# Kernel tuning notes

Measured on AMD Instinct MI355X. Metric: run time of the kernel, lower is better.

## Reference

```python
import jax, jax.numpy as jnp
import numpy as np
from jax import lax

B, S, H, T = 64, 512, 1024, 17


def setup_inputs() -> dict:
    key = jax.random.key(0)
    ks = jax.random.split(key, 7)
    x = jax.random.normal(ks[0], (B, S, H), dtype=jnp.float32)
    W = jax.random.normal(ks[1], (T, H), dtype=jnp.float32) * 0.02
    b = jax.random.normal(ks[2], (T,), dtype=jnp.float32) * 0.02
    transitions = jax.random.normal(ks[3], (T, T), dtype=jnp.float32)
    start_trans = jax.random.normal(ks[4], (T,), dtype=jnp.float32)
    end_trans = jax.random.normal(ks[5], (T,), dtype=jnp.float32)
    nwords = jax.random.randint(ks[6], (B,), 1, S + 1, dtype=jnp.int32)
    return {"x": x, "W": W, "b": b, "transitions": transitions,
            "start_trans": start_trans, "end_trans": end_trans, "nwords": nwords}


def _viterbi(feats, mask_bs, transitions, start_trans, end_trans):
    # feats: [B,S,T]; mask_bs: [B,S] bool. Returns best tag sequence [B,S] (int32).
    Bt, St, Tt = feats.shape
    init = start_trans[None, :] + feats[:, 0]  # [B,T]
    idT = jnp.arange(Tt, dtype=jnp.int32)

    def step(score, inp):
        f_t, m_t = inp  # [B,T], [B]
        cand = score[:, :, None] + transitions[None, :, :]      # [B,Tprev,Tcur]
        best = jnp.max(cand, axis=1) + f_t                      # [B,T]
        bp = jnp.argmax(cand, axis=1).astype(jnp.int32)         # [B,T]
        m = m_t[:, None]
        new_score = jnp.where(m, best, score)
        bp = jnp.where(m, bp, idT[None, :])                     # identity where padded
        return new_score, bp

    xs = (jnp.swapaxes(feats[:, 1:], 0, 1), jnp.swapaxes(mask_bs[:, 1:], 0, 1))
    final, bps = lax.scan(step, init, xs)                       # bps: [S-1,B,T]
    final = final + end_trans[None, :]
    last_tag = jnp.argmax(final, axis=1).astype(jnp.int32)      # [B]

    def back(tag, bp_t):
        prev = jnp.take_along_axis(bp_t, tag[:, None], axis=1)[:, 0]
        return prev, tag

    first_tag, later_tags = lax.scan(back, last_tag, bps, reverse=True)
    tags = jnp.concatenate([first_tag[:, None], jnp.swapaxes(later_tags, 0, 1)], axis=1)  # [B,S]
    return tags


def reference(x, W, b, transitions, start_trans, end_trans, nwords):
    # dropout p=0.0 -> identity
    feats = jnp.einsum('bsh,th->bst', x, W) + b                 # hidden2tag
    mask_bs = jnp.arange(feats.shape[1])[None, :] < nwords[:, None]
    tags = _viterbi(feats, mask_bs, transitions, start_trans, end_trans)
    padded_tags = jnp.where(mask_bs, tags, 0).astype(jnp.float32)  # pad=0, float dtype
    return padded_tags, feats
```

## Files before the change

### kernel.cpp

```cpp
#include <hip/hip_runtime.h>

#define HDIM 1024
#define TDIM 17
#define BDIM 64
#define SDIM 512
#define NROWS (BDIM * SDIM)
#define NCH 8
#define CHL 64

__global__ __launch_bounds__(256) void gemm_kernel(
    const float* __restrict__ x, const float* __restrict__ W,
    const float* __restrict__ bias, float* __restrict__ feats) {
  __shared__ __align__(16) float sW[TDIM * 512];
  int tid = threadIdx.x;
  int sub = tid & 15;
  int g = tid >> 4;
  int row0 = blockIdx.x * 32 + g * 2;
  const float* xr = x + (size_t)row0 * HDIM;
  float acc[2][TDIM];
#pragma unroll
  for (int r = 0; r < 2; ++r)
#pragma unroll
    for (int t = 0; t < TDIM; ++t) acc[r][t] = 0.f;

  for (int ph = 0; ph < 2; ++ph) {
    if (ph) __syncthreads();
    for (int i = tid; i < TDIM * 128; i += 256) {
      int t = i >> 7;
      int k = (i & 127) * 4;
      *(float4*)&sW[t * 512 + k] =
          *(const float4*)&W[(size_t)t * HDIM + ph * 512 + k];
    }
    __syncthreads();
    float4 xv[2], xn[2];
#pragma unroll
    for (int r = 0; r < 2; ++r)
      xv[r] = *(const float4*)(xr + r * HDIM + ph * 512 + sub * 4);
#pragma unroll
    for (int c = 0; c < 8; ++c) {
      if (c < 7) {
#pragma unroll
        for (int r = 0; r < 2; ++r)
          xn[r] =
              *(const float4*)(xr + r * HDIM + ph * 512 + (c + 1) * 64 + sub * 4);
      }
#pragma unroll
      for (int t = 0; t < TDIM; ++t) {
        float4 wv = *(const float4*)&sW[t * 512 + c * 64 + sub * 4];
#pragma unroll
        for (int r = 0; r < 2; ++r) {
          float a = acc[r][t];
          a = fmaf(xv[r].x, wv.x, a);
          a = fmaf(xv[r].y, wv.y, a);
          a = fmaf(xv[r].z, wv.z, a);
          a = fmaf(xv[r].w, wv.w, a);
          acc[r][t] = a;
        }
      }
#pragma unroll
      for (int r = 0; r < 2; ++r) xv[r] = xn[r];
    }
  }
#pragma unroll
  for (int r = 0; r < 2; ++r)
#pragma unroll
    for (int t = 0; t < TDIM; ++t) {
#pragma unroll
      for (int m = 1; m < 16; m <<= 1)
        acc[r][t] += __shfl_xor(acc[r][t], m, 64);
    }
#pragma unroll
  for (int r = 0; r < 2; ++r) {
    float val = acc[r][0];
#pragma unroll
    for (int t = 1; t < 16; ++t) val = (sub == t) ? acc[r][t] : val;
    feats[(size_t)(row0 + r) * TDIM + sub] = val + bias[sub];
    if (sub == 0)
      feats[(size_t)(row0 + r) * TDIM + 16] = acc[r][16] + bias[16];
  }
}

__device__ __forceinline__ float vmax17(const float* v) {
  float m0 = fmaxf(fmaxf(v[0], v[1]), v[2]);
  float m1 = fmaxf(fmaxf(v[3], v[4]), v[5]);
  float m2 = fmaxf(fmaxf(v[6], v[7]), v[8]);
  float m3 = fmaxf(fmaxf(v[9], v[10]), v[11]);
  float m4 = fmaxf(fmaxf(v[12], v[13]), v[14]);
  float m5 = fmaxf(v[15], v[16]);
  float n0 = fmaxf(fmaxf(m0, m1), m2);
  float n1 = fmaxf(fmaxf(m3, m4), m5);
  return fmaxf(n0, n1);
}

__global__ __launch_bounds__(384) void chunkprod_kernel(
    const float* __restrict__ feats, const float* __restrict__ trans,
    const int* __restrict__ nwords, float* __restrict__ Pbuf) {
  int bc = blockIdx.x;
  int b = bc >> 3, c = bc & 7;
  int nw = nwords[b];
  if (nw < 1) nw = 1;
  if (nw > SDIM) nw = SDIM;
  if (c > 0 && c * CHL > nw - 1) return;
  int tid = threadIdx.x;
  int wid = tid >> 6, lane = tid & 63;
  int g = lane / 17, j = lane % 17;
  int gc = g < 3 ? g : 2;
  int e = wid * 3 + gc;
  int ibase = gc * 17 * 4;
  const float* fb = feats + (size_t)b * SDIM * TDIM;
  float tcol[TDIM];
#pragma unroll
  for (int i = 0; i < TDIM; ++i) tcol[i] = trans[i * TDIM + j];
  float s = (j == e) ? 0.f : -1e30f;
  int t_start = (c == 0) ? 1 : c * CHL;
  int t_end = c * CHL + CHL - 1;
  if (t_end > nw - 1) t_end = nw - 1;
  int tA = t_start;
  int tB = t_start + 1;
  if (tB > t_end) tB = t_start;
  float fA = fb[(size_t)tA * TDIM + j];
  float fB = fb[(size_t)tB * TDIM + j];
  for (int t = t_start; t <= t_end; ++t) {
    int t2 = t + 2;
    if (t2 > t_end) t2 = t_end;
    float fC = fb[(size_t)t2 * TDIM + j];
    int sb = __float_as_int(s);
    float v[TDIM];
#pragma unroll
    for (int i = 0; i < TDIM; ++i)
      v[i] = __int_as_float(__builtin_amdgcn_ds_bpermute(ibase + 4 * i, sb)) +
             tcol[i];
    float maxv = vmax17(v);
    s = maxv + fA;
    fA = fB;
    fB = fC;
  }
  if (g < 3 && e < TDIM)
    Pbuf[((size_t)(b * NCH + c) * TDIM + e) * TDIM + j] = s;
}

__global__ __launch_bounds__(64) void scan_kernel(
    const float* __restrict__ feats, const float* __restrict__ start_t,
    const float* __restrict__ end_t, const int* __restrict__ nwords,
    const float* __restrict__ Pbuf, float* __restrict__ bnd,
    int* __restrict__ elast) {
  int b = blockIdx.x;
  int lane = threadIdx.x;
  int jj = lane < TDIM ? lane : TDIM - 1;
  int nw = nwords[b];
  if (nw < 1) nw = 1;
  if (nw > SDIM) nw = SDIM;
  int clast = (nw - 1) >> 6;
  float w = start_t[jj] + feats[(size_t)b * SDIM * TDIM + jj];
  for (int c = 0; c <= clast; ++c) {
    const float* Pc = Pbuf + (size_t)(b * NCH + c) * TDIM * TDIM;
    float pj[TDIM];
#pragma unroll
    for (int i = 0; i < TDIM; ++i) pj[i] = Pc[i * TDIM + jj];
    int wb = __float_as_int(w);
    float v[TDIM];
#pragma unroll
    for (int i = 0; i < TDIM; ++i)
      v[i] = __int_as_float(__builtin_amdgcn_ds_bpermute(4 * i, wb)) + pj[i];
    w = vmax17(v);
    if (lane < TDIM) bnd[(b * NCH + c) * TDIM + lane] = w;
  }
  float fin = w + end_t[jj];
  float tmax = (lane < TDIM) ? fin : -1e30f;
#pragma unroll
  for (int m = 1; m < 64; m <<= 1) tmax = fmaxf(tmax, __shfl_xor(tmax, m, 64));
  unsigned long long mm = __ballot(fin == tmax) & 0x1FFFFull;
  if (lane == 0) elast[b] = (int)(__ffsll((unsigned long long)mm) - 1);
}

__global__ __launch_bounds__(64) void rerun_kernel(
    const float* __restrict__ feats, const float* __restrict__ trans,
    const float* __restrict__ start_t, const int* __restrict__ nwords,
    const float* __restrict__ bnd, int* __restrict__ etag,
    unsigned* __restrict__ seq32) {
  __shared__ unsigned char s_bp[CHL * 20];
  __shared__ __align__(4) unsigned char s_seq[TDIM * 68];
  int bc = blockIdx.x;
  int b = bc >> 3, c = bc & 7;
  int nw = nwords[b];
  if (nw < 1) nw = 1;
  if (nw > SDIM) nw = SDIM;
  if (c > 0 && c * CHL > nw - 1) return;
  int lane = threadIdx.x;
  int jj = lane < TDIM ? lane : TDIM - 1;
  const float* fb = feats + (size_t)b * SDIM * TDIM;
  float tcol[TDIM];
#pragma unroll
  for (int i = 0; i < TDIM; ++i) tcol[i] = trans[i * TDIM + jj];
  float sj = (c == 0) ? (start_t[jj] + fb[jj])
                      : bnd[(b * NCH + c - 1) * TDIM + jj];
  int t_start = (c == 0) ? 1 : c * CHL;
  int t_end = c * CHL + CHL - 1;
  if (t_end > nw - 1) t_end = nw - 1;
  int tA = t_start;
  int tB = t_start + 1;
  if (tB > t_end) tB = t_start;
  float fA = fb[(size_t)tA * TDIM + jj];
  float fB = fb[(size_t)tB * TDIM + jj];
  for (int t = t_start; t <= t_end; ++t) {
    int t2 = t + 2;
    if (t2 > t_end) t2 = t_end;
    float fC = fb[(size_t)t2 * TDIM + jj];
    int sb = __float_as_int(sj);
    float v[TDIM];
#pragma unroll
    for (int i = 0; i < TDIM; ++i)
      v[i] = __int_as_float(__builtin_amdgcn_ds_bpermute(4 * i, sb)) + tcol[i];
    float maxv = vmax17(v);
    unsigned msk = 0;
#pragma unroll
    for (int i = 0; i < TDIM; ++i) msk |= (v[i] == maxv) ? (1u << i) : 0u;
    int bp = __ffs(msk) - 1;
    s_bp[(t - c * CHL) * 20 + jj] = (unsigned char)bp;
    sj = maxv + fA;
    fA = fB;
    fB = fC;
  }
  __syncthreads();
  if (lane < TDIM) {
    int tag = lane;
    for (int t = t_end; t >= t_start; --t) {
      int u = t - c * CHL;
      s_seq[lane * 68 + u] = (unsigned char)tag;
      tag = s_bp[u * 20 + tag];
    }
    if (c == 0)
      s_seq[lane * 68 + 0] = (unsigned char)tag;
    else
      etag[(b * NCH + c) * TDIM + lane] = tag;
  }
  __syncthreads();
  for (int i = lane; i < TDIM * 16; i += 64) {
    int e2 = i >> 4, q = i & 15;
    seq32[(((size_t)(b * NCH + c) * TDIM + e2) << 4) + q] =
        *(const unsigned*)&s_seq[e2 * 68 + q * 4];
  }
}

__global__ __launch_bounds__(64) void stitch_kernel(
    const int* __restrict__ nwords, const int* __restrict__ elast,
    const int* __restrict__ etag, const unsigned* __restrict__ seq32,
    float* __restrict__ tags_out) {
  __shared__ unsigned long long stz[64];
  int b = blockIdx.x;
  int lane = threadIdx.x;
  int nw = nwords[b];
  if (nw < 1) nw = 1;
  if (nw > SDIM) nw = SDIM;
  stz[lane] = 0ull;
  __syncthreads();
  unsigned char* st = (unsigned char*)stz;
  int clast = (nw - 1) >> 6;
  int e = elast[b];
  for (int c = clast; c >= 0; --c) {
    int t_end = c * CHL + CHL - 1;
    if (t_end > nw - 1) t_end = nw - 1;
    int u_end = t_end - c * CHL;
    if (lane < 16) {
      unsigned wv = seq32[(((size_t)(b * NCH + c) * TDIM + e) << 4) + lane];
#pragma unroll
      for (int z = 0; z < 4; ++z) {
        int u = lane * 4 + z;
        if (u <= u_end) st[c * CHL + u] = (wv >> (8 * z)) & 0xff;
      }
    }
    if (c > 0) e = etag[(b * NCH + c) * TDIM + e];
  }
  __syncthreads();
  float* ob = tags_out + (size_t)b * SDIM;
  for (int t = lane; t < SDIM; t += 64)
    ob[t] = (t < nw) ? (float)st[t] : 0.f;
}

#define TRS 20
#define MVC 136

__global__ __launch_bounds__(64) void viterbi_kernel(
    const float* __restrict__ feats, const float* __restrict__ trans,
    const float* __restrict__ start_t, const float* __restrict__ end_t,
    const int* __restrict__ nwords, float* __restrict__ tags_out) {
  __shared__ __align__(16) float s_mv[64 * MVC];
  __shared__ float s_tr[TDIM * TRS];
  __shared__ unsigned char s_tags[SDIM];
  int b = blockIdx.x;
  int lane = threadIdx.x;
  const float* fb = feats + (size_t)b * SDIM * TDIM;
  for (int i = lane; i < TDIM * TDIM; i += 64)
    s_tr[(i / TDIM) * TRS + (i % TDIM)] = trans[i];
  __syncthreads();
  int nw = nwords[b];
  if (nw < 1) nw = 1;
  if (nw > SDIM) nw = SDIM;
  int jj = lane < TDIM ? lane : TDIM - 1;
  float tcol[TDIM];
#pragma unroll
  for (int i = 0; i < TDIM; ++i) tcol[i] = trans[i * TDIM + jj];
  float s[TDIM];
#pragma unroll
  for (int i = 0; i < TDIM; ++i) s[i] = start_t[i] + fb[i];
  float s0reg = start_t[jj] + fb[jj];
  auto load8g = [&](float* f, int t) {
#pragma unroll
    for (int u = 0; u < 8; ++u) f[u] = fb[(size_t)(t + u) * TDIM + jj];
  };
  auto step = [&](float fcu) -> float {
    float v[TDIM];
#pragma unroll
    for (int i = 0; i < TDIM; ++i) v[i] = s[i] + tcol[i];
    float maxv = vmax17(v);
    float ns = maxv + fcu;
#pragma unroll
    for (int i = 0; i < TDIM; ++i)
      s[i] = __uint_as_float(
          (unsigned)__builtin_amdgcn_readlane((int)__float_as_uint(ns), i));
    return maxv;
  };
  float fc[8], fn[8], mvr[8];
  load8g(fc, 0);
  {
    load8g(fn, 8);
    mvr[0] = 0.f;
#pragma unroll
    for (int u = 1; u < 8; ++u) {
      mvr[u] = 0.f;
      if (u < nw) mvr[u] = step(fc[u]);
    }
    if (lane < TDIM) {
      *(float4*)&s_mv[lane * 8] = make_float4(mvr[0], mvr[1], mvr[2], mvr[3]);
      *(float4*)&s_mv[lane * 8 + 4] =
          make_float4(mvr[4], mvr[5], mvr[6], mvr[7]);
    }
#pragma unroll
    for (int u = 0; u < 8; ++u) fc[u] = fn[u];
  }
  int t0 = 8;
  for (; t0 + 8 <= nw; t0 += 8) {
    int tn = (t0 + 8 <= SDIM - 8) ? t0 + 8 : t0;
    load8g(fn, tn);
#pragma unroll
    for (int u = 0; u < 8; ++u) mvr[u] = step(fc[u]);
    int cb = (t0 >> 3) * MVC;
    if (lane < TDIM) {
      *(float4*)&s_mv[cb + lane * 8] =
          make_float4(mvr[0], mvr[1], mvr[2], mvr[3]);
      *(float4*)&s_mv[cb + lane * 8 + 4] =
          make_float4(mvr[4], mvr[5], mvr[6], mvr[7]);
    }
#pragma unroll
    for (int u = 0; u < 8; ++u) fc[u] = fn[u];
  }
  if (t0 < nw) {
#pragma unroll
    for (int u = 0; u < 8; ++u) {
      mvr[u] = 0.f;
      if (t0 + u < nw) mvr[u] = step(fc[u]);
    }
    int cb = (t0 >> 3) * MVC;
    if (lane < TDIM) {
      *(float4*)&s_mv[cb + lane * 8] =
          make_float4(mvr[0], mvr[1], mvr[2], mvr[3]);
      *(float4*)&s_mv[cb + lane * 8 + 4] =
          make_float4(mvr[4], mvr[5], mvr[6], mvr[7]);
    }
  }
  float bv = s[0] + end_t[0];
  int bi = 0;
#pragma unroll
  for (int j = 1; j < TDIM; ++j) {
    float cc = s[j] + end_t[j];
    bool p = cc > bv;
    bv = p ? cc : bv;
    bi = p ? j : bi;
  }
  int tag = __builtin_amdgcn_readfirstlane(bi);
  s_tags[nw - 1] = (unsigned char)tag;
  {
    int t = nw - 1;
    int ip = t - 1 > 0 ? t - 1 : 0;
    float fv = fb[(size_t)ip * TDIM + jj];
    float mvv = s_mv[(ip >> 3) * MVC + jj * 8 + (ip & 7)];
    while (t >= 1) {
      float tr = s_tr[jj * TRS + tag];
      float target = s_mv[(t >> 3) * MVC + tag * 8 + (t & 7)];
      int inx = t - 2 > 0 ? t - 2 : 0;
      float fvn = fb[(size_t)inx * TDIM + jj];
      float mvn = s_mv[(inx >> 3) * MVC + jj * 8 + (inx & 7)];
      float sv = (t - 1 == 0) ? s0reg : (mvv + fv);
      float cand = sv + tr;
      unsigned long long m = __ballot(cand == target) & 0x1FFFFull;
      tag = __ffsll(m) - 1;
      s_tags[t - 1] = (unsigned char)tag;
      fv = fvn;
      mvv = mvn;
      --t;
    }
  }
  __syncthreads();
  float* ob = tags_out + (size_t)b * SDIM;
  for (int t = lane; t < SDIM; t += 64)
    ob[t] = (t < nw) ? (float)s_tags[t] : 0.f;
}

extern "C" void kernel_launch(void* const* d_in, const int* in_sizes, int n_in,
                              void* d_out, int out_size, void* d_ws,
                              size_t ws_size, hipStream_t stream) {
  const float* x = (const float*)d_in[0];
  const float* W = (const float*)d_in[1];
  const float* b = (const float*)d_in[2];
  const float* trans = (const float*)d_in[3];
  const float* start_t = (const float*)d_in[4];
  const float* end_t = (const float*)d_in[5];
  const int* nwords = (const int*)d_in[6];
  float* out = (float*)d_out;
  float* tags_out = out;
  float* feats_out = out + NROWS;

  gemm_kernel<<<NROWS / 32, 256, 0, stream>>>(x, W, b, feats_out);

  if (ws_size >= (size_t)1218816 && d_ws != nullptr) {
    char* ws = (char*)d_ws;
    float* Pbuf = (float*)(ws);
    float* bnd = (float*)(ws + 591872);
    int* elast = (int*)(ws + 626688);
    int* etag = (int*)(ws + 626944);
    unsigned* seq32 = (unsigned*)(ws + 661760);
    chunkprod_kernel<<<BDIM * NCH, 384, 0, stream>>>(feats_out, trans, nwords,
                                                     Pbuf);
    scan_kernel<<<BDIM, 64, 0, stream>>>(feats_out, start_t, end_t, nwords,
                                         Pbuf, bnd, elast);
    rerun_kernel<<<BDIM * NCH, 64, 0, stream>>>(feats_out, trans, start_t,
                                                nwords, bnd, etag, seq32);
    stitch_kernel<<<BDIM, 64, 0, stream>>>(nwords, elast, etag, seq32,
                                           tags_out);
  } else {
    viterbi_kernel<<<BDIM, 64, 0, stream>>>(feats_out, trans, start_t, end_t,
                                            nwords, tags_out);
  }
}
```

Before: 287.4 us.

## Fuse Viterbi scan, rerun and stitch into one block; deepen GEMM x prefetch

Merges the scan, per-chunk rerun/backtrack and stitch kernels into one 512-thread kernel per batch row. Chunk boundary scores, backpointer sequences and end tags now stay in shared memory, which removes two launches and the global-memory round trips between them. Each wave handles one chunk after wave 0 finishes the sequential chunk-product scan. Separately, the GEMM now keeps a 4-deep rolling register prefetch of x float4s instead of a 1-deep one, raising register use in exchange for better latency hiding.

Measured after the change: 393.8 us. +37.0%, slower.

```diff
diff --git a/kernel.cpp b/kernel.cpp
--- a/kernel.cpp
+++ b/kernel.cpp
@@ -23,6 +23,13 @@
 #pragma unroll
     for (int t = 0; t < TDIM; ++t) acc[r][t] = 0.f;
 
+  float4 xb[4][2];
+#pragma unroll
+  for (int d = 0; d < 4; ++d)
+#pragma unroll
+    for (int r = 0; r < 2; ++r)
+      xb[d][r] = *(const float4*)(xr + r * HDIM + d * 64 + sub * 4);
+
   for (int ph = 0; ph < 2; ++ph) {
     if (ph) __syncthreads();
     for (int i = tid; i < TDIM * 128; i += 256) {
@@ -32,17 +39,17 @@
           *(const float4*)&W[(size_t)t * HDIM + ph * 512 + k];
     }
     __syncthreads();
-    float4 xv[2], xn[2];
-#pragma unroll
-    for (int r = 0; r < 2; ++r)
-      xv[r] = *(const float4*)(xr + r * HDIM + ph * 512 + sub * 4);
 #pragma unroll
     for (int c = 0; c < 8; ++c) {
-      if (c < 7) {
+      int cc = ph * 8 + c;
+      float4 xv[2];
+#pragma unroll
+      for (int r = 0; r < 2; ++r) xv[r] = xb[cc & 3][r];
+      if (cc + 4 < 16) {
 #pragma unroll
         for (int r = 0; r < 2; ++r)
-          xn[r] =
-              *(const float4*)(xr + r * HDIM + ph * 512 + (c + 1) * 64 + sub * 4);
+          xb[cc & 3][r] =
+              *(const float4*)(xr + r * HDIM + (cc + 4) * 64 + sub * 4);
       }
 #pragma unroll
       for (int t = 0; t < TDIM; ++t) {
@@ -57,8 +64,6 @@
           acc[r][t] = a;
         }
       }
-#pragma unroll
-      for (int r = 0; r < 2; ++r) xv[r] = xn[r];
     }
   }
 #pragma unroll
@@ -139,142 +144,119 @@
     Pbuf[((size_t)(b * NCH + c) * TDIM + e) * TDIM + j] = s;
 }
 
-__global__ __launch_bounds__(64) void scan_kernel(
-    const float* __restrict__ feats, const float* __restrict__ start_t,
-    const float* __restrict__ end_t, const int* __restrict__ nwords,
-    const float* __restrict__ Pbuf, float* __restrict__ bnd,
-    int* __restrict__ elast) {
+__global__ __launch_bounds__(512) void viterbi_tail_kernel(
+    const float* __restrict__ feats, const float* __restrict__ trans,
+    const float* __restrict__ start_t, const float* __restrict__ end_t,
+    const int* __restrict__ nwords, const float* __restrict__ Pbuf,
+    float* __restrict__ tags_out) {
+  __shared__ float s_bnd[NCH][TDIM];
+  __shared__ unsigned char s_bp[NCH][CHL][20];
+  __shared__ unsigned char s_seq[NCH][TDIM][68];
+  __shared__ int s_etag[NCH][TDIM];
+  __shared__ int s_chosen[NCH];
+  __shared__ int s_elast;
   int b = blockIdx.x;
-  int lane = threadIdx.x;
-  int jj = lane < TDIM ? lane : TDIM - 1;
+  int tid = threadIdx.x;
+  int wid = tid >> 6, lane = tid & 63;
   int nw = nwords[b];
   if (nw < 1) nw = 1;
   if (nw > SDIM) nw = SDIM;
-  int clast = (nw - 1) >> 6;
-  float w = start_t[jj] + feats[(size_t)b * SDIM * TDIM + jj];
-  for (int c = 0; c <= clast; ++c) {
-    const float* Pc = Pbuf + (size_t)(b * NCH + c) * TDIM * TDIM;
-    float pj[TDIM];
-#pragma unroll
-    for (int i = 0; i < TDIM; ++i) pj[i] = Pc[i * TDIM + jj];
-    int wb = __float_as_int(w);
-    float v[TDIM];
-#pragma unroll
-    for (int i = 0; i < TDIM; ++i)
-      v[i] = __int_as_float(__builtin_amdgcn_ds_bpermute(4 * i, wb)) + pj[i];
-    w = vmax17(v);
-    if (lane < TDIM) bnd[(b * NCH + c) * TDIM + lane] = w;
-  }
-  float fin = w + end_t[jj];
-  float tmax = (lane < TDIM) ? fin : -1e30f;
-#pragma unroll
-  for (int m = 1; m < 64; m <<= 1) tmax = fmaxf(tmax, __shfl_xor(tmax, m, 64));
-  unsigned long long mm = __ballot(fin == tmax) & 0x1FFFFull;
-  if (lane == 0) elast[b] = (int)(__ffsll((unsigned long long)mm) - 1);
-}
-
-__global__ __launch_bounds__(64) void rerun_kernel(
-    const float* __restrict__ feats, const float* __restrict__ trans,
-    const float* __restrict__ start_t, const int* __restrict__ nwords,
-    const float* __restrict__ bnd, int* __restrict__ etag,
-    unsigned* __restrict__ seq32) {
-  __shared__ unsigned char s_bp[CHL * 20];
-  __shared__ __align__(4) unsigned char s_seq[TDIM * 68];
-  int bc = blockIdx.x;
-  int b = bc >> 3, c = bc & 7;
-  int nw = nwords[b];
-  if (nw < 1) nw = 1;
-  if (nw > SDIM) nw = SDIM;
-  if (c > 0 && c * CHL > nw - 1) return;
-  int lane = threadIdx.x;
   int jj = lane < TDIM ? lane : TDIM - 1;
   const float* fb = feats + (size_t)b * SDIM * TDIM;
-  float tcol[TDIM];
-#pragma unroll
-  for (int i = 0; i < TDIM; ++i) tcol[i] = trans[i * TDIM + jj];
-  float sj = (c == 0) ? (start_t[jj] + fb[jj])
-                      : bnd[(b * NCH + c - 1) * TDIM + jj];
+  int clast = (nw - 1) >> 6;
+
+  if (wid == 0) {
+    float w = start_t[jj] + fb[jj];
+    for (int c = 0; c <= clast; ++c) {
+      const float* Pc = Pbuf + (size_t)(b * NCH + c) * TDIM * TDIM;
+      float pj[TDIM];
+#pragma unroll
+      for (int i = 0; i < TDIM; ++i) pj[i] = Pc[i * TDIM + jj];
+      int wb = __float_as_int(w);
+      float v[TDIM];
+#pragma unroll
+      for (int i = 0; i < TDIM; ++i)
+        v[i] = __int_as_float(__builtin_amdgcn_ds_bpermute(4 * i, wb)) + pj[i];
+      w = vmax17(v);
+      if (lane < TDIM) s_bnd[c][lane] = w;
+    }
+    float fin = w + end_t[jj];
+    float tmax = (lane < TDIM) ? fin : -1e30f;
+#pragma unroll
+    for (int m = 1; m < 64; m <<= 1)
+      tmax = fmaxf(tmax, __shfl_xor(tmax, m, 64));
+    unsigned long long mm = __ballot(fin == tmax) & 0x1FFFFull;
+    if (lane == 0) s_elast = (int)(__ffsll(mm) - 1);
+  }
+  __syncthreads();
+
+  int c = wid;
+  bool active = (c == 0) || (c * CHL <= nw - 1);
   int t_start = (c == 0) ? 1 : c * CHL;
   int t_end = c * CHL + CHL - 1;
   if (t_end > nw - 1) t_end = nw - 1;
-  int tA = t_start;
-  int tB = t_start + 1;
-  if (tB > t_end) tB = t_start;
-  float fA = fb[(size_t)tA * TDIM + jj];
-  float fB = fb[(size_t)tB * TDIM + jj];
-  for (int t = t_start; t <= t_end; ++t) {
-    int t2 = t + 2;
-    if (t2 > t_end) t2 = t_end;
-    float fC = fb[(size_t)t2 * TDIM + jj];
-    int sb = __float_as_int(sj);
-    float v[TDIM];
-#pragma unroll
-    for (int i = 0; i < TDIM; ++i)
-      v[i] = __int_as_float(__builtin_amdgcn_ds_bpermute(4 * i, sb)) + tcol[i];
-    float maxv = vmax17(v);
-    unsigned msk = 0;
-#pragma unroll
-    for (int i = 0; i < TDIM; ++i) msk |= (v[i] == maxv) ? (1u << i) : 0u;
-    int bp = __ffs(msk) - 1;
-    s_bp[(t - c * CHL) * 20 + jj] = (unsigned char)bp;
-    sj = maxv + fA;
-    fA = fB;
-    fB = fC;
-  }
-  __syncthreads();
-  if (lane < TDIM) {
+  if (active) {
+    float tcol[TDIM];
+#pragma unroll
+    for (int i = 0; i < TDIM; ++i) tcol[i] = trans[i * TDIM + jj];
+    float sj = (c == 0) ? (start_t[jj] + fb[jj]) : s_bnd[c - 1][jj];
+    int tA = t_start;
+    int tB = t_start + 1;
+    if (tB > t_end) tB = t_start;
+    float fA = fb[(size_t)tA * TDIM + jj];
+    float fB = fb[(size_t)tB * TDIM + jj];
+    for (int t = t_start; t <= t_end; ++t) {
+      int t2 = t + 2;
+      if (t2 > t_end) t2 = t_end;
+      float fC = fb[(size_t)t2 * TDIM + jj];
+      int sb = __float_as_int(sj);
+      float v[TDIM];
+#pragma unroll
+      for (int i = 0; i < TDIM; ++i)
+        v[i] =
+            __int_as_float(__builtin_amdgcn_ds_bpermute(4 * i, sb)) + tcol[i];
+      float maxv = vmax17(v);
+      unsigned msk = 0;
+#pragma unroll
+      for (int i = 0; i < TDIM; ++i) msk |= (v[i] == maxv) ? (1u << i) : 0u;
+      int bp = __ffs(msk) - 1;
+      s_bp[c][t - c * CHL][jj] = (unsigned char)bp;
+      sj = maxv + fA;
+      fA = fB;
+      fB = fC;
+    }
+  }
+  __syncthreads();
+
+  if (active && lane < TDIM) {
     int tag = lane;
     for (int t = t_end; t >= t_start; --t) {
       int u = t - c * CHL;
-      s_seq[lane * 68 + u] = (unsigned char)tag;
-      tag = s_bp[u * 20 + tag];
+      s_seq[c][lane][u] = (unsigned char)tag;
+      tag = s_bp[c][u][tag];
     }
     if (c == 0)
-      s_seq[lane * 68 + 0] = (unsigned char)tag;
+      s_seq[0][lane][0] = (unsigned char)tag;
     else
-      etag[(b * NCH + c) * TDIM + lane] = tag;
-  }
-  __syncthreads();
-  for (int i = lane; i < TDIM * 16; i += 64) {
-    int e2 = i >> 4, q = i & 15;
-    seq32[(((size_t)(b * NCH + c) * TDIM + e2) << 4) + q] =
-        *(const unsigned*)&s_seq[e2 * 68 + q * 4];
-  }
-}
-
-__global__ __launch_bounds__(64) void stitch_kernel(
-    const int* __restrict__ nwords, const int* __restrict__ elast,
-    const int* __restrict__ etag, const unsigned* __restrict__ seq32,
-    float* __restrict__ tags_out) {
-  __shared__ unsigned long long stz[64];
-  int b = blockIdx.x;
-  int lane = threadIdx.x;
-  int nw = nwords[b];
-  if (nw < 1) nw = 1;
-  if (nw > SDIM) nw = SDIM;
-  stz[lane] = 0ull;
-  __syncthreads();
-  unsigned char* st = (unsigned char*)stz;
-  int clast = (nw - 1) >> 6;
-  int e = elast[b];
-  for (int c = clast; c >= 0; --c) {
-    int t_end = c * CHL + CHL - 1;
-    if (t_end > nw - 1) t_end = nw - 1;
-    int u_end = t_end - c * CHL;
-    if (lane < 16) {
-      unsigned wv = seq32[(((size_t)(b * NCH + c) * TDIM + e) << 4) + lane];
-#pragma unroll
-      for (int z = 0; z < 4; ++z) {
-        int u = lane * 4 + z;
-        if (u <= u_end) st[c * CHL + u] = (wv >> (8 * z)) & 0xff;
-      }
-    }
-    if (c > 0) e = etag[(b * NCH + c) * TDIM + e];
-  }
-  __syncthreads();
-  float* ob = tags_out + (size_t)b * SDIM;
-  for (int t = lane; t < SDIM; t += 64)
-    ob[t] = (t < nw) ? (float)st[t] : 0.f;
+      s_etag[c][lane] = tag;
+  }
+  __syncthreads();
+
+  if (tid == 0) {
+    int e = s_elast;
+    for (int c2 = clast; c2 >= 0; --c2) {
+      s_chosen[c2] = e;
+      if (c2 > 0) e = s_etag[c2][e];
+    }
+  }
+  __syncthreads();
+  int t = tid;
+  float val = 0.f;
+  if (t < nw) {
+    int c2 = t >> 6, u = t & 63;
+    val = (float)s_seq[c2][s_chosen[c2]][u];
+  }
+  tags_out[(size_t)b * SDIM + t] = val;
 }
 
 #define TRS 20
@@ -422,21 +404,12 @@
 
   gemm_kernel<<<NROWS / 32, 256, 0, stream>>>(x, W, b, feats_out);
 
-  if (ws_size >= (size_t)1218816 && d_ws != nullptr) {
-    char* ws = (char*)d_ws;
-    float* Pbuf = (float*)(ws);
-    float* bnd = (float*)(ws + 591872);
-    int* elast = (int*)(ws + 626688);
-    int* etag = (int*)(ws + 626944);
-    unsigned* seq32 = (unsigned*)(ws + 661760);
+  if (ws_size >= (size_t)591872 && d_ws != nullptr) {
+    float* Pbuf = (float*)d_ws;
     chunkprod_kernel<<<BDIM * NCH, 384, 0, stream>>>(feats_out, trans, nwords,
                                                      Pbuf);
-    scan_kernel<<<BDIM, 64, 0, stream>>>(feats_out, start_t, end_t, nwords,
-                                         Pbuf, bnd, elast);
-    rerun_kernel<<<BDIM * NCH, 64, 0, stream>>>(feats_out, trans, start_t,
-                                                nwords, bnd, etag, seq32);
-    stitch_kernel<<<BDIM, 64, 0, stream>>>(nwords, elast, etag, seq32,
-                                           tags_out);
+    viterbi_tail_kernel<<<BDIM, 512, 0, stream>>>(
+        feats_out, trans, start_t, end_t, nwords, Pbuf, tags_out);
   } else {
     viterbi_kernel<<<BDIM, 64, 0, stream>>>(feats_out, trans, start_t, end_t,
                                             nwords, tags_out);
```
